# Optimization experiments

Measured on AMD Instinct MI355X. Metric: run time of the kernel, lower is better.

## Reference

```python
import jax, jax.numpy as jnp
import numpy as np

N = 50000      # nodes
E = 800000     # edges (avg degree 16)
DIN = 64       # input feature dim
DOUT = 64      # output feature dim
NSLOPE = 0.2   # LeakyReLU negative slope


def setup_inputs() -> dict:
    key = jax.random.key(0)
    k1, k2, k3, k4 = jax.random.split(key, 4)
    x = jax.random.normal(k1, (N, DIN), dtype=jnp.float32)
    W = jax.random.normal(k2, (DOUT, DIN), dtype=jnp.float32) * (1.0 / np.sqrt(DIN))
    b = jnp.zeros((DOUT,), dtype=jnp.float32)
    a = jax.random.normal(k3, (DOUT,), dtype=jnp.float32) * (1.0 / np.sqrt(DOUT))
    edge_index = jax.random.randint(k4, (2, E), 0, N, dtype=jnp.int32)
    return {"x": x, "W": W, "b": b, "a": a, "edge_index": edge_index}


def reference(x, W, b, a, edge_index):
    # GATv2: e_ij = a^T LeakyReLU(W h_i + W h_j + b); softmax over incoming
    # neighbors j of node i; h_i' = sigmoid(sum_j alpha_ij * W h_j)
    Wh = x @ W.T + b                          # [N, DOUT]
    src, dst = edge_index[0], edge_index[1]   # edge j -> i
    s = Wh[dst] + Wh[src]                     # [E, DOUT] per-edge pre-activation
    e = jnp.where(s > 0, s, NSLOPE * s) @ a   # [E] attention logits
    # numerically stable segment softmax over destination nodes
    emax = jax.ops.segment_max(e, dst, num_segments=N)       # [N]
    emax = jnp.where(jnp.isfinite(emax), emax, 0.0)          # nodes with no edges
    ex = jnp.exp(e - emax[dst])                               # [E]
    denom = jax.ops.segment_sum(ex, dst, num_segments=N)      # [N]
    alpha = ex / jnp.maximum(denom[dst], 1e-9)                # [E]
    agg = jax.ops.segment_sum(alpha[:, None] * Wh[src], dst, num_segments=N)
    return jax.nn.sigmoid(agg)                # [N, DOUT]
```

## Files before the change

### kernel.cpp

```cpp
#include <hip/hip_runtime.h>
#include <hip/hip_bf16.h>
#include <math.h>

#define NN 50000
#define EE 800000
#define DD 64
#define NSLOPE 0.2f
#define NBUCK 196
#define CAP 4608
#define CHUNK 2048
#define BINB ((EE + CHUNK - 1) / CHUNK)
#define WHB 782

__device__ __forceinline__ float leaky(float s) { return s > 0.f ? s : NSLOPE * s; }

__global__ void __launch_bounds__(256) bin_kernel(
    const int* __restrict__ ei, unsigned int* __restrict__ gbuf,
    int* __restrict__ gCursor) {
    __shared__ int cnt[256];
    __shared__ int excl[256];
    __shared__ int cur[256];
    __shared__ int base[256];
    __shared__ unsigned int pairs[CHUNK];
    int tid = threadIdx.x;
    int start = blockIdx.x * CHUNK;
    int nedge = min(CHUNK, EE - start);
    cnt[tid] = 0; cur[tid] = 0;
    __syncthreads();
    for (int j = 0; j < CHUNK / 256; ++j) {
        int i = start + tid + j * 256;
        if (i < EE) atomicAdd(&cnt[((unsigned int)ei[EE + i]) >> 8], 1);
    }
    __syncthreads();
    int v = cnt[tid];
    excl[tid] = v; __syncthreads();
    for (int o = 1; o < 256; o <<= 1) {
        int t = (tid >= o) ? excl[tid - o] : 0;
        __syncthreads();
        excl[tid] += t;
        __syncthreads();
    }
    int ex = excl[tid] - v;
    __syncthreads();
    excl[tid] = ex;
    __syncthreads();
    for (int j = 0; j < CHUNK / 256; ++j) {
        int i = start + tid + j * 256;
        if (i < EE) {
            unsigned int src = (unsigned int)ei[i];
            unsigned int dst = (unsigned int)ei[EE + i];
            int b = dst >> 8;
            int r = atomicAdd(&cur[b], 1);
            pairs[excl[b] + r] = (dst << 16) | src;
        }
    }
    if (tid < NBUCK) base[tid] = atomicAdd(&gCursor[tid], cnt[tid]);
    __syncthreads();
    for (int i = tid; i < nedge; i += 256) {
        unsigned int p = pairs[i];
        int b = p >> 24;
        gbuf[(size_t)b * CAP + base[b] + (i - excl[b])] = p;
    }
}

__global__ void __launch_bounds__(256) csr_wh_kernel(
    const unsigned int* __restrict__ gbuf, const int* __restrict__ gCursor,
    int* __restrict__ off, unsigned short* __restrict__ csr,
    const float* __restrict__ x, const float* __restrict__ W,
    const float* __restrict__ bias, float* __restrict__ Wh) {
    __shared__ __align__(16) char smem[20480];
    int tid = threadIdx.x;

    if (blockIdx.x < NBUCK) {
        int* s    = (int*)smem;
        int* hist = s + 256;
        int* excl = s + 512;
        int* cur  = s + 768;
        int k = blockIdx.x;
        int v = (tid < NBUCK) ? gCursor[tid] : 0;
        s[tid] = v; __syncthreads();
        for (int o = 1; o < 256; o <<= 1) {
            int t = (tid >= o) ? s[tid - o] : 0;
            __syncthreads();
            s[tid] += t;
            __syncthreads();
        }
        int base_k = (k == 0) ? 0 : s[k - 1];
        int cnt = s[k] - base_k;
        const unsigned int* bp = gbuf + (size_t)k * CAP;
        hist[tid] = 0; cur[tid] = 0;
        __syncthreads();
        for (int i = tid; i < cnt; i += 256)
            atomicAdd(&hist[(bp[i] >> 16) & 255], 1);
        __syncthreads();
        int hv = hist[tid];
        excl[tid] = hv; __syncthreads();
        for (int o = 1; o < 256; o <<= 1) {
            int t = (tid >= o) ? excl[tid - o] : 0;
            __syncthreads();
            excl[tid] += t;
            __syncthreads();
        }
        int hex = excl[tid] - hv;
        __syncthreads();
        excl[tid] = hex;
        __syncthreads();
        int dst = k * 256 + tid;
        if (dst < NN) off[dst] = base_k + hex;
        if (k == 0 && tid == 0) off[NN] = EE;
        for (int i = tid; i < cnt; i += 256) {
            unsigned int p = bp[i];
            int local = (p >> 16) & 255;
            int slot = base_k + excl[local] + atomicAdd(&cur[local], 1);
            csr[slot] = (unsigned short)(p & 0xffffu);
        }
        return;
    }

    int bid = blockIdx.x - NBUCK;
    float4* Wl = (float4*)smem;
    float4 (*xr)[4][16] = (float4 (*)[4][16])(smem + 16384);
    const float4* W4 = (const float4*)W;
    const float4* x4 = (const float4*)x;
    for (int i = tid; i < 1024; i += 256) {
        int c = i >> 4, k4 = i & 15;
        Wl[c * 16 + (k4 ^ (c & 15))] = W4[i];
    }
    __syncthreads();
    int wv = tid >> 6, lane = tid & 63;
    int c = lane;
    float4 wreg[16];
#pragma unroll
    for (int k4 = 0; k4 < 16; ++k4) wreg[k4] = Wl[c * 16 + (k4 ^ (c & 15))];
    float bv = bias[c];
    int l16 = lane >> 4, q = lane & 15;
    for (int rowbase = (bid * 4 + wv) * 4; rowbase < NN; rowbase += WHB * 16) {
        xr[wv][l16][q] = x4[(size_t)(rowbase + l16) * 16 + q];
        float acc0 = bv, acc1 = bv, acc2 = bv, acc3 = bv;
#pragma unroll
        for (int k4 = 0; k4 < 16; ++k4) {
            float4 w  = wreg[k4];
            float4 q0 = xr[wv][0][k4];
            float4 q1 = xr[wv][1][k4];
            float4 q2 = xr[wv][2][k4];
            float4 q3 = xr[wv][3][k4];
            acc0 += w.x * q0.x + w.y * q0.y + w.z * q0.z + w.w * q0.w;
            acc1 += w.x * q1.x + w.y * q1.y + w.z * q1.z + w.w * q1.w;
            acc2 += w.x * q2.x + w.y * q2.y + w.z * q2.z + w.w * q2.w;
            acc3 += w.x * q3.x + w.y * q3.y + w.z * q3.z + w.w * q3.w;
        }
        Wh[(size_t)(rowbase + 0) * DD + c] = acc0;
        Wh[(size_t)(rowbase + 1) * DD + c] = acc1;
        Wh[(size_t)(rowbase + 2) * DD + c] = acc2;
        Wh[(size_t)(rowbase + 3) * DD + c] = acc3;
    }
}

__global__ void __launch_bounds__(256) fused_kernel(
    const float4* __restrict__ Wh4, const float4* __restrict__ a4,
    const int* __restrict__ off, const unsigned short* __restrict__ csr,
    float4* __restrict__ out4) {
    int wave = threadIdx.x >> 6, lane = threadIdx.x & 63;
    int node = blockIdx.x * 4 + wave;
    int b = lane >> 4, f4 = lane & 15;
    float4 av  = a4[f4];
    float4 whi = Wh4[(size_t)node * 16 + f4];
    int beg = off[node], end = off[node + 1];
    float den = 0.f;
    float4 acc = make_float4(0.f, 0.f, 0.f, 0.f);
    float4 p0 = make_float4(0.f, 0.f, 0.f, 0.f);
    float4 p1 = make_float4(0.f, 0.f, 0.f, 0.f);
    if (beg < end) {
        int i0 = beg + b;
        int s0 = csr[(i0 < end) ? i0 : (end - 1)];
        p0 = Wh4[(size_t)s0 * 16 + f4];
        int i1 = beg + 4 + b;
        if (i1 < end) {
            int s1 = csr[i1];
            p1 = Wh4[(size_t)s1 * 16 + f4];
        }
    }
    for (int base = beg; base < end; base += 4) {
        float4 whs = p0;
        p0 = p1;
        int ni = base + 8 + b;
        if (ni < end) {
            int s2 = csr[ni];
            p1 = Wh4[(size_t)s2 * 16 + f4];
        }
        float t = av.x * leaky(whi.x + whs.x) + av.y * leaky(whi.y + whs.y)
                + av.z * leaky(whi.z + whs.z) + av.w * leaky(whi.w + whs.w);
        t += __shfl_xor(t, 1, 64);
        t += __shfl_xor(t, 2, 64);
        t += __shfl_xor(t, 4, 64);
        t += __shfl_xor(t, 8, 64);
        float ex = (base + b < end) ? __expf(t) : 0.f;
        den += ex;
        acc.x += ex * whs.x; acc.y += ex * whs.y;
        acc.z += ex * whs.z; acc.w += ex * whs.w;
    }
    acc.x += __shfl_xor(acc.x, 16, 64); acc.y += __shfl_xor(acc.y, 16, 64);
    acc.z += __shfl_xor(acc.z, 16, 64); acc.w += __shfl_xor(acc.w, 16, 64);
    den   += __shfl_xor(den,   16, 64);
    acc.x += __shfl_xor(acc.x, 32, 64); acc.y += __shfl_xor(acc.y, 32, 64);
    acc.z += __shfl_xor(acc.z, 32, 64); acc.w += __shfl_xor(acc.w, 32, 64);
    den   += __shfl_xor(den,   32, 64);
    if (b == 0) {
        float id = 1.f / fmaxf(den, 1e-9f);
        float4 o;
        o.x = 1.f / (1.f + __expf(-acc.x * id));
        o.y = 1.f / (1.f + __expf(-acc.y * id));
        o.z = 1.f / (1.f + __expf(-acc.z * id));
        o.w = 1.f / (1.f + __expf(-acc.w * id));
        out4[(size_t)node * 16 + f4] = o;
    }
}

extern "C" void kernel_launch(void* const* d_in, const int* in_sizes, int n_in,
                              void* d_out, int out_size, void* d_ws, size_t ws_size,
                              hipStream_t stream) {
    const float* x = (const float*)d_in[0];
    const float* W = (const float*)d_in[1];
    const float* b = (const float*)d_in[2];
    const float* a = (const float*)d_in[3];
    const int*   ei = (const int*)d_in[4];
    float* out = (float*)d_out;

    char* ws = (char*)d_ws;
    float*          Wh      = (float*)(ws);
    int*            gCursor = (int*)(ws + 12800000);
    int*            off     = (int*)(ws + 12801024);
    unsigned int*   gbuf    = (unsigned int*)(ws + 13001216);
    unsigned short* csr     = (unsigned short*)(ws + 16613888);

    hipMemsetAsync(gCursor, 0, 1024, stream);
    bin_kernel<<<BINB, 256, 0, stream>>>(ei, gbuf, gCursor);
    csr_wh_kernel<<<NBUCK + WHB, 256, 0, stream>>>(gbuf, gCursor, off, csr,
                                                   x, W, b, Wh);
    fused_kernel<<<NN / 4, 256, 0, stream>>>((const float4*)Wh, (const float4*)a,
                                             off, csr, (float4*)out);
}
```

Measured before the change: 142.4 us.

## Co-schedule Wh projection with edge binning and clamp prefetch indices in aggregation

Moves the dense Wh projection out of the CSR-build kernel and into the binning kernel, so the projection blocks run alongside the edge-binning blocks. The CSR build becomes its own small kernel of NBUCK blocks. In the aggregation kernel, prefetch loads now use indices clamped to the last edge instead of branches, which removes divergent conditionals but re-reads the last neighbour row. The goal is to overlap the compute-bound projection with the scatter-bound binning and to shorten the critical path before the fused kernel.

```diff
diff --git a/kernel.cpp b/kernel.cpp
--- a/kernel.cpp
+++ b/kernel.cpp
@@ -14,110 +14,62 @@
 
 __device__ __forceinline__ float leaky(float s) { return s > 0.f ? s : NSLOPE * s; }
 
-__global__ void __launch_bounds__(256) bin_kernel(
+__global__ void __launch_bounds__(256) bin_wh_kernel(
     const int* __restrict__ ei, unsigned int* __restrict__ gbuf,
-    int* __restrict__ gCursor) {
-    __shared__ int cnt[256];
-    __shared__ int excl[256];
-    __shared__ int cur[256];
-    __shared__ int base[256];
-    __shared__ unsigned int pairs[CHUNK];
-    int tid = threadIdx.x;
-    int start = blockIdx.x * CHUNK;
-    int nedge = min(CHUNK, EE - start);
-    cnt[tid] = 0; cur[tid] = 0;
-    __syncthreads();
-    for (int j = 0; j < CHUNK / 256; ++j) {
-        int i = start + tid + j * 256;
-        if (i < EE) atomicAdd(&cnt[((unsigned int)ei[EE + i]) >> 8], 1);
-    }
-    __syncthreads();
-    int v = cnt[tid];
-    excl[tid] = v; __syncthreads();
-    for (int o = 1; o < 256; o <<= 1) {
-        int t = (tid >= o) ? excl[tid - o] : 0;
-        __syncthreads();
-        excl[tid] += t;
-        __syncthreads();
-    }
-    int ex = excl[tid] - v;
-    __syncthreads();
-    excl[tid] = ex;
-    __syncthreads();
-    for (int j = 0; j < CHUNK / 256; ++j) {
-        int i = start + tid + j * 256;
-        if (i < EE) {
-            unsigned int src = (unsigned int)ei[i];
-            unsigned int dst = (unsigned int)ei[EE + i];
-            int b = dst >> 8;
-            int r = atomicAdd(&cur[b], 1);
-            pairs[excl[b] + r] = (dst << 16) | src;
-        }
-    }
-    if (tid < NBUCK) base[tid] = atomicAdd(&gCursor[tid], cnt[tid]);
-    __syncthreads();
-    for (int i = tid; i < nedge; i += 256) {
-        unsigned int p = pairs[i];
-        int b = p >> 24;
-        gbuf[(size_t)b * CAP + base[b] + (i - excl[b])] = p;
-    }
-}
-
-__global__ void __launch_bounds__(256) csr_wh_kernel(
-    const unsigned int* __restrict__ gbuf, const int* __restrict__ gCursor,
-    int* __restrict__ off, unsigned short* __restrict__ csr,
+    int* __restrict__ gCursor,
     const float* __restrict__ x, const float* __restrict__ W,
     const float* __restrict__ bias, float* __restrict__ Wh) {
     __shared__ __align__(16) char smem[20480];
     int tid = threadIdx.x;
 
-    if (blockIdx.x < NBUCK) {
-        int* s    = (int*)smem;
-        int* hist = s + 256;
-        int* excl = s + 512;
-        int* cur  = s + 768;
-        int k = blockIdx.x;
-        int v = (tid < NBUCK) ? gCursor[tid] : 0;
-        s[tid] = v; __syncthreads();
-        for (int o = 1; o < 256; o <<= 1) {
-            int t = (tid >= o) ? s[tid - o] : 0;
-            __syncthreads();
-            s[tid] += t;
-            __syncthreads();
-        }
-        int base_k = (k == 0) ? 0 : s[k - 1];
-        int cnt = s[k] - base_k;
-        const unsigned int* bp = gbuf + (size_t)k * CAP;
-        hist[tid] = 0; cur[tid] = 0;
-        __syncthreads();
-        for (int i = tid; i < cnt; i += 256)
-            atomicAdd(&hist[(bp[i] >> 16) & 255], 1);
-        __syncthreads();
-        int hv = hist[tid];
-        excl[tid] = hv; __syncthreads();
+    if (blockIdx.x < BINB) {
+        int* cnt  = (int*)smem;
+        int* excl = cnt + 256;
+        int* cur  = cnt + 512;
+        int* base = cnt + 768;
+        unsigned int* pairs = (unsigned int*)(smem + 4096);
+        int start = blockIdx.x * CHUNK;
+        int nedge = min(CHUNK, EE - start);
+        cnt[tid] = 0; cur[tid] = 0;
+        __syncthreads();
+        for (int j = 0; j < CHUNK / 256; ++j) {
+            int i = start + tid + j * 256;
+            if (i < EE) atomicAdd(&cnt[((unsigned int)ei[EE + i]) >> 8], 1);
+        }
+        __syncthreads();
+        int v = cnt[tid];
+        excl[tid] = v; __syncthreads();
         for (int o = 1; o < 256; o <<= 1) {
             int t = (tid >= o) ? excl[tid - o] : 0;
             __syncthreads();
             excl[tid] += t;
             __syncthreads();
         }
-        int hex = excl[tid] - hv;
-        __syncthreads();
-        excl[tid] = hex;
-        __syncthreads();
-        int dst = k * 256 + tid;
-        if (dst < NN) off[dst] = base_k + hex;
-        if (k == 0 && tid == 0) off[NN] = EE;
-        for (int i = tid; i < cnt; i += 256) {
-            unsigned int p = bp[i];
-            int local = (p >> 16) & 255;
-            int slot = base_k + excl[local] + atomicAdd(&cur[local], 1);
-            csr[slot] = (unsigned short)(p & 0xffffu);
+        int ex = excl[tid] - v;
+        __syncthreads();
+        excl[tid] = ex;
+        __syncthreads();
+        for (int j = 0; j < CHUNK / 256; ++j) {
+            int i = start + tid + j * 256;
+            if (i < EE) {
+                unsigned int src = (unsigned int)ei[i];
+                unsigned int dst = (unsigned int)ei[EE + i];
+                int bk = dst >> 8;
+                int r = atomicAdd(&cur[bk], 1);
+                pairs[excl[bk] + r] = (dst << 16) | src;
+            }
+        }
+        if (tid < NBUCK) base[tid] = atomicAdd(&gCursor[tid], cnt[tid]);
+        __syncthreads();
+        for (int i = tid; i < nedge; i += 256) {
+            unsigned int p = pairs[i];
+            int bk = p >> 24;
+            gbuf[(size_t)bk * CAP + base[bk] + (i - excl[bk])] = p;
         }
         return;
     }
 
-    int bid = blockIdx.x - NBUCK;
+    int bid = blockIdx.x - BINB;
     float4* Wl = (float4*)smem;
     float4 (*xr)[4][16] = (float4 (*)[4][16])(smem + 16384);
     const float4* W4 = (const float4*)W;
@@ -156,6 +108,54 @@
     }
 }
 
+__global__ void __launch_bounds__(256) csr_kernel(
+    const unsigned int* __restrict__ gbuf, const int* __restrict__ gCursor,
+    int* __restrict__ off, unsigned short* __restrict__ csr) {
+    __shared__ int s[256];
+    __shared__ int hist[256];
+    __shared__ int excl[256];
+    __shared__ int cur[256];
+    int tid = threadIdx.x;
+    int k = blockIdx.x;
+    int v = (tid < NBUCK) ? gCursor[tid] : 0;
+    s[tid] = v; __syncthreads();
+    for (int o = 1; o < 256; o <<= 1) {
+        int t = (tid >= o) ? s[tid - o] : 0;
+        __syncthreads();
+        s[tid] += t;
+        __syncthreads();
+    }
+    int base_k = (k == 0) ? 0 : s[k - 1];
+    int cnt = s[k] - base_k;
+    const unsigned int* bp = gbuf + (size_t)k * CAP;
+    hist[tid] = 0; cur[tid] = 0;
+    __syncthreads();
+    for (int i = tid; i < cnt; i += 256)
+        atomicAdd(&hist[(bp[i] >> 16) & 255], 1);
+    __syncthreads();
+    int hv = hist[tid];
+    excl[tid] = hv; __syncthreads();
+    for (int o = 1; o < 256; o <<= 1) {
+        int t = (tid >= o) ? excl[tid - o] : 0;
+        __syncthreads();
+        excl[tid] += t;
+        __syncthreads();
+    }
+    int hex = excl[tid] - hv;
+    __syncthreads();
+    excl[tid] = hex;
+    __syncthreads();
+    int dst = k * 256 + tid;
+    if (dst < NN) off[dst] = base_k + hex;
+    if (k == 0 && tid == 0) off[NN] = EE;
+    for (int i = tid; i < cnt; i += 256) {
+        unsigned int p = bp[i];
+        int local = (p >> 16) & 255;
+        int slot = base_k + excl[local] + atomicAdd(&cur[local], 1);
+        csr[slot] = (unsigned short)(p & 0xffffu);
+    }
+}
+
 __global__ void __launch_bounds__(256) fused_kernel(
     const float4* __restrict__ Wh4, const float4* __restrict__ a4,
     const int* __restrict__ off, const unsigned short* __restrict__ csr,
@@ -168,36 +168,28 @@
     int beg = off[node], end = off[node + 1];
     float den = 0.f;
     float4 acc = make_float4(0.f, 0.f, 0.f, 0.f);
-    float4 p0 = make_float4(0.f, 0.f, 0.f, 0.f);
-    float4 p1 = make_float4(0.f, 0.f, 0.f, 0.f);
     if (beg < end) {
-        int i0 = beg + b;
-        int s0 = csr[(i0 < end) ? i0 : (end - 1)];
-        p0 = Wh4[(size_t)s0 * 16 + f4];
-        int i1 = beg + 4 + b;
-        if (i1 < end) {
-            int s1 = csr[i1];
-            p1 = Wh4[(size_t)s1 * 16 + f4];
-        }
-    }
-    for (int base = beg; base < end; base += 4) {
-        float4 whs = p0;
-        p0 = p1;
-        int ni = base + 8 + b;
-        if (ni < end) {
-            int s2 = csr[ni];
-            p1 = Wh4[(size_t)s2 * 16 + f4];
-        }
-        float t = av.x * leaky(whi.x + whs.x) + av.y * leaky(whi.y + whs.y)
-                + av.z * leaky(whi.z + whs.z) + av.w * leaky(whi.w + whs.w);
-        t += __shfl_xor(t, 1, 64);
-        t += __shfl_xor(t, 2, 64);
-        t += __shfl_xor(t, 4, 64);
-        t += __shfl_xor(t, 8, 64);
-        float ex = (base + b < end) ? __expf(t) : 0.f;
-        den += ex;
-        acc.x += ex * whs.x; acc.y += ex * whs.y;
-        acc.z += ex * whs.z; acc.w += ex * whs.w;
+        int last = end - 1;
+        int i0 = min(beg + b, last);
+        int i1 = min(beg + 4 + b, last);
+        float4 p0 = Wh4[(size_t)csr[i0] * 16 + f4];
+        float4 p1 = Wh4[(size_t)csr[i1] * 16 + f4];
+        for (int base = beg; base < end; base += 4) {
+            float4 whs = p0;
+            p0 = p1;
+            int ni = min(base + 8 + b, last);
+            p1 = Wh4[(size_t)csr[ni] * 16 + f4];
+            float t = av.x * leaky(whi.x + whs.x) + av.y * leaky(whi.y + whs.y)
+                    + av.z * leaky(whi.z + whs.z) + av.w * leaky(whi.w + whs.w);
+            t += __shfl_xor(t, 1, 64);
+            t += __shfl_xor(t, 2, 64);
+            t += __shfl_xor(t, 4, 64);
+            t += __shfl_xor(t, 8, 64);
+            float ex = (base + b < end) ? __expf(t) : 0.f;
+            den += ex;
+            acc.x += ex * whs.x; acc.y += ex * whs.y;
+            acc.z += ex * whs.z; acc.w += ex * whs.w;
+        }
     }
     acc.x += __shfl_xor(acc.x, 16, 64); acc.y += __shfl_xor(acc.y, 16, 64);
     acc.z += __shfl_xor(acc.z, 16, 64); acc.w += __shfl_xor(acc.w, 16, 64);
@@ -234,9 +226,8 @@
     unsigned short* csr     = (unsigned short*)(ws + 16613888);
 
     hipMemsetAsync(gCursor, 0, 1024, stream);
-    bin_kernel<<<BINB, 256, 0, stream>>>(ei, gbuf, gCursor);
-    csr_wh_kernel<<<NBUCK + WHB, 256, 0, stream>>>(gbuf, gCursor, off, csr,
-                                                   x, W, b, Wh);
+    bin_wh_kernel<<<BINB + WHB, 256, 0, stream>>>(ei, gbuf, gCursor, x, W, b, Wh);
+    csr_kernel<<<NBUCK, 256, 0, stream>>>(gbuf, gCursor, off, csr);
     fused_kernel<<<NN / 4, 256, 0, stream>>>((const float4*)Wh, (const float4*)a,
                                              off, csr, (float4*)out);
 }
```

After: 146.6 us. 3.0% more time.
